# Optimization experiments

Hardware: AMD Instinct MI355X
Metric: run time of the kernel (lower is better)

## Reference

```python
import jax, jax.numpy as jnp
import numpy as np

B, S, H = 1, 2048, 4096
NH, NKV, HD = 32, 8, 128
GROUP = NH // NKV  # 4
SCALE = 0.08838834764831845  # 1/sqrt(head_dim)
ROPE_BASE = 10000.0


def setup_inputs() -> dict:
    key = jax.random.key(0)
    k1, k2, k3 = jax.random.split(key, 3)
    hidden_states = jax.random.normal(k1, (B, S, H), jnp.float32)
    # c_attn: [H + 2*NKV*HD, H] = [6144, 4096]; c_proj: [H, H]
    w_attn = jax.random.normal(k2, (H + 2 * NKV * HD, H), jnp.float32) * 0.02
    w_proj = jax.random.normal(k3, (H, H), jnp.float32) * (0.02 / np.sqrt(2 * 32))
    # standard rotate-half RoPE tables, shape [S, HD]
    inv_freq = 1.0 / (ROPE_BASE ** (jnp.arange(0, HD, 2, dtype=jnp.float32) / HD))
    freqs = jnp.outer(jnp.arange(S, dtype=jnp.float32), inv_freq)
    emb = jnp.concatenate([freqs, freqs], axis=-1)
    return {
        "hidden_states": hidden_states,
        "w_attn": w_attn,
        "w_proj": w_proj,
        "rope_cos": jnp.cos(emb),
        "rope_sin": jnp.sin(emb),
    }


def _apply_rope(x, cos, sin):
    # x: [B, heads, S, HD]; cos/sin: [S, HD] broadcast over batch/heads
    x1, x2 = jnp.split(x, 2, axis=-1)
    rot = jnp.concatenate([-x2, x1], axis=-1)
    return x * cos + rot * sin


def reference(hidden_states, w_attn, w_proj, rope_cos, rope_sin):
    b, s, _ = hidden_states.shape
    # fused QKV projection (no bias)
    qkv = hidden_states @ w_attn.T  # [B, S, H + 2*NKV*HD]
    qkv = qkv.reshape(b, s, NKV, (GROUP + 2) * HD)
    q = qkv[..., : GROUP * HD].reshape(b, s, NH, HD)
    k = qkv[..., GROUP * HD : (GROUP + 1) * HD]  # [B, S, NKV, HD]
    v = qkv[..., (GROUP + 1) * HD :]
    q = q.transpose(0, 2, 1, 3)  # [B, NH, S, HD]
    k = k.transpose(0, 2, 1, 3)  # [B, NKV, S, HD]
    v = v.transpose(0, 2, 1, 3)
    q = _apply_rope(q, rope_cos, rope_sin)
    k = _apply_rope(k, rope_cos, rope_sin)
    # GQA: group query heads per kv head instead of repeating K/V
    qg = q.reshape(b, NKV, GROUP, s, HD)
    scores = jnp.einsum("bkgqd,bksd->bkgqs", qg, k) * SCALE
    causal = jnp.tril(jnp.ones((s, s), dtype=bool))
    scores = jnp.where(causal, scores, jnp.finfo(scores.dtype).min)
    probs = jax.nn.softmax(scores, axis=-1)
    out = jnp.einsum("bkgqs,bksd->bkgqd", probs, v)
    out = out.reshape(b, NH, s, HD).transpose(0, 2, 1, 3).reshape(b, s, NH * HD)
    return out @ w_proj.T
```

## Files before the change

kernel.cpp:

```cpp
#include <hip/hip_runtime.h>
#include <cstdint>
#include <cstddef>

typedef __attribute__((ext_vector_type(4))) float f32x4;
typedef __attribute__((ext_vector_type(8))) short bf16x8;

#define S_LEN 2048
#define HDIM 4096
#define QKVD 6144
#define NHEAD 32
#define NKVH 8
#define HD 128
#define ATT_SCALE 0.08838834764831845f

__device__ __forceinline__ short f2bf(float f) {
  unsigned int u = __float_as_uint(f);
  u += 0x7FFFu + ((u >> 16) & 1u);
  return (short)(u >> 16);
}

__device__ __forceinline__ void gl_lds16(const short* g, short* l) {
  __builtin_amdgcn_global_load_lds((const __attribute__((address_space(1))) void*)g,
                                   (__attribute__((address_space(3))) void*)l,
                                   16, 0, 0);
}

template<int N> __device__ __forceinline__ void vmw() {
  if constexpr (N == 0) asm volatile("s_waitcnt vmcnt(0)" ::: "memory");
  else if constexpr (N == 1) asm volatile("s_waitcnt vmcnt(1)" ::: "memory");
  else if constexpr (N == 2) asm volatile("s_waitcnt vmcnt(2)" ::: "memory");
  else if constexpr (N == 3) asm volatile("s_waitcnt vmcnt(3)" ::: "memory");
  else if constexpr (N == 4) asm volatile("s_waitcnt vmcnt(4)" ::: "memory");
}

__global__ void cvt_kernel(const float* __restrict__ in, short* __restrict__ out, int n) {
  int i = (blockIdx.x * blockDim.x + threadIdx.x) * 4;
  if (i >= n) return;
  const float4 v = *reinterpret_cast<const float4*>(in + i);
  short4 o;
  o.x = f2bf(v.x); o.y = f2bf(v.y); o.z = f2bf(v.z); o.w = f2bf(v.w);
  *reinterpret_cast<short4*>(out + i) = o;
}

#define PHASEX(MH, NH, VM, STAGE) { \
    bf16x8 af[2][2], bfr[NQ][2]; \
    { const short* bA = lA + buf * ATILE; const short* bB = lB + buf * BTILE; \
      _Pragma("unroll") for (int m = 0; m < 2; ++m) { \
        int row = wm * 64 + (MH) * 32 + m * 16 + l15; \
        _Pragma("unroll") for (int kk = 0; kk < 2; ++kk) { \
          int slot = ((kk << 2) + l4) ^ (row & 7); \
          af[m][kk] = *reinterpret_cast<const bf16x8*>(bA + row * 64 + slot * 8); } } \
      _Pragma("unroll") for (int n = 0; n < NQ; ++n) { \
        int row = wn * (BN >> 2) + n * 32 + (NH) * 16 + l15; \
        _Pragma("unroll") for (int kk = 0; kk < 2; ++kk) { \
          int slot = ((kk << 2) + l4) ^ (row & 7); \
          bfr[n][kk] = *reinterpret_cast<const bf16x8*>(bB + row * 64 + slot * 8); } } } \
    STAGE; \
    vmw<(VM)>(); \
    __builtin_amdgcn_s_barrier(); \
    __builtin_amdgcn_sched_barrier(0); \
    __builtin_amdgcn_s_setprio(1); \
    _Pragma("unroll") for (int m = 0; m < 2; ++m) \
      _Pragma("unroll") for (int n = 0; n < NQ; ++n) \
        _Pragma("unroll") for (int kk = 0; kk < 2; ++kk) \
          acc[(MH) * 2 + m][(NH) * NQ + n] = __builtin_amdgcn_mfma_f32_16x16x32_bf16( \
              af[m][kk], bfr[n][kk], acc[(MH) * 2 + m][(NH) * NQ + n], 0, 0, 0); \
    __builtin_amdgcn_s_setprio(0); }

template<int BN>
__global__ __launch_bounds__(512, 2) void gemm8p(const short* __restrict__ A,
                                                 const short* __restrict__ B,
                                                 float* __restrict__ C,
                                                 int M, int N, int K) {
  extern __shared__ short sm[];
  constexpr int NQ = BN / 128;
  constexpr int ATILE = 128 * 64;
  constexpr int BTILE = BN * 64;
  const int tid = threadIdx.x;
  const int wv = tid >> 6, lane = tid & 63;
  const int wm = wv >> 2, wn = wv & 3;
  const int l15 = lane & 15, l4 = lane >> 4;
  const int nbn = N / BN;
  const int nwg = gridDim.x;
  const int bid = blockIdx.x;
  const int sbid = (bid & 7) * (nwg >> 3) + (bid >> 3);
  const int tm = (sbid / nbn) * 128, tn = (sbid % nbn) * BN;
  short* lA = sm;
  short* lB = sm + 2 * ATILE;
  (void)M;

  f32x4 acc[4][2 * NQ] = {};

  auto stageA = [&](int k0, int bufi, int sel) {
    short* dst = lA + bufi * ATILE;
    int rowIdx = tid >> 3;
    int row = (rowIdx >> 5) * 64 + sel * 32 + (rowIdx & 31);
    int slot = tid & 7;
    gl_lds16(A + (size_t)(tm + row) * K + k0 + ((slot ^ (row & 7)) << 3),
             dst + row * 64 + slot * 8);
  };
  auto stageB = [&](int k0, int bufi, int par) {
    short* dst = lB + bufi * BTILE;
#pragma unroll
    for (int j = 0; j < NQ; ++j) {
      int rowIdx = (tid >> 3) + j * 64;
      int row = (rowIdx >> 4) * 32 + par * 16 + (rowIdx & 15);
      int slot = tid & 7;
      gl_lds16(B + (size_t)(tn + row) * K + k0 + ((slot ^ (row & 7)) << 3),
               dst + row * 64 + slot * 8);
    }
  };

  stageA(0, 0, 0);
  stageB(0, 0, 0);
  stageB(0, 0, 1);
  stageA(0, 0, 1);
  vmw<NQ + 1>();
  __builtin_amdgcn_s_barrier();
  __builtin_amdgcn_sched_barrier(0);

  const int KT = K >> 6;
  for (int t = 0; t < KT - 1; ++t) {
    const int buf = t & 1, nbuf = buf ^ 1, nk0 = (t + 1) << 6;
    PHASEX(0, 0, 2,      stageA(nk0, nbuf, 0))
    PHASEX(0, 1, NQ + 1, stageB(nk0, nbuf, 0))
    PHASEX(1, 0, 99,     stageB(nk0, nbuf, 1))
    PHASEX(1, 1, NQ + 1, stageA(nk0, nbuf, 1))
  }
  {
    const int buf = (KT - 1) & 1;
    PHASEX(0, 0, 1,  (void)0)
    PHASEX(0, 1, 0,  (void)0)
    PHASEX(1, 0, 99, (void)0)
    PHASEX(1, 1, 99, (void)0)
  }
#pragma unroll
  for (int mg = 0; mg < 4; ++mg)
#pragma unroll
    for (int NH = 0; NH < 2; ++NH)
#pragma unroll
      for (int n = 0; n < NQ; ++n)
#pragma unroll
        for (int r = 0; r < 4; ++r) {
          int row = tm + wm * 64 + mg * 16 + l4 * 4 + r;
          int col = tn + wn * (BN >> 2) + n * 32 + NH * 16 + l15;
          C[(size_t)row * N + col] = acc[mg][NH * NQ + n][r];
        }
}

__global__ void rope2_kernel(const float* __restrict__ qkv,
                             const float* __restrict__ cb,
                             const float* __restrict__ sb,
                             short* __restrict__ Q,
                             short* __restrict__ Kx) {
  int tid = blockIdx.x * blockDim.x + threadIdx.x;
  int dh = tid & 63;
  int t2 = tid >> 6;
  int part = t2 % 5;
  int t3 = t2 / 5;
  int g = t3 & 7;
  int s = t3 >> 3;
  const float* base = qkv + (size_t)s * QKVD + g * 768 + part * 128;
  float v1 = base[dh], v2 = base[dh + 64];
  float c = cb[s * HD + dh], sn = sb[s * HD + dh];
  float o1 = v1 * c - v2 * sn;
  float o2 = v2 * c + v1 * sn;
  short* dst = (part < 4) ? (Q + ((size_t)(g * 4 + part) * S_LEN + s) * HD)
                          : (Kx + ((size_t)g * S_LEN + s) * HD);
  dst[dh] = f2bf(o1);
  dst[dh + 64] = f2bf(o2);
}

__global__ __launch_bounds__(256) void vtrans2_kernel(const float* __restrict__ qkv,
                                                      short* __restrict__ Vt) {
  __shared__ short tile[64][72];
  const int kvh = blockIdx.z;
  const int s0 = blockIdx.x * 64, d0 = blockIdx.y * 64;
  const int t = threadIdx.x;
#pragma unroll
  for (int i = 0; i < 4; ++i) {
    int c = t + i * 256;
    int sl = c >> 4, dl = (c & 15) * 4;
    const float4 v = *reinterpret_cast<const float4*>(
        qkv + (size_t)(s0 + sl) * QKVD + kvh * 768 + 640 + d0 + dl);
    tile[sl][dl] = f2bf(v.x); tile[sl][dl + 1] = f2bf(v.y);
    tile[sl][dl + 2] = f2bf(v.z); tile[sl][dl + 3] = f2bf(v.w);
  }
  __syncthreads();
  short* Vtb = Vt + (size_t)kvh * HD * S_LEN;
#pragma unroll
  for (int i = 0; i < 2; ++i) {
    int dl = i * 32 + (t >> 3), sl = (t & 7) * 8;
    bf16x8 o;
#pragma unroll
    for (int j = 0; j < 8; ++j) o[j] = tile[sl + j][dl];
    *reinterpret_cast<bf16x8*>(Vtb + (size_t)(d0 + dl) * S_LEN + s0 + sl) = o;
  }
}

__global__ __launch_bounds__(256, 2) void attn_kernel(const short* __restrict__ Q,
                                                      const short* __restrict__ Kx,
                                                      const short* __restrict__ Vt,
                                                      short* __restrict__ AO) {
  __shared__ short lK[2 * 64 * 128];
  __shared__ unsigned int lPu[4 * 2 * 512];
  const int tt = threadIdx.x;
  const int w = tt >> 6, lane = tt & 63;
  const int l15 = lane & 15, l4 = lane >> 4;
  const int kvh = blockIdx.x;
  const int y = blockIdx.y;
  const int qt = (y < 32) ? (2 * y) : (127 - 2 * y);
  const int h = kvh * 4 + w;

  bf16x8 qf[2][4];
#pragma unroll
  for (int qa = 0; qa < 2; ++qa) {
    const short* qrow = Q + ((size_t)h * S_LEN + qt * 32 + qa * 16 + l15) * HD + l4 * 8;
#pragma unroll
    for (int fd = 0; fd < 4; ++fd)
      qf[qa][fd] = *reinterpret_cast<const bf16x8*>(qrow + fd * 32);
  }

  f32x4 o[2][8] = {};
  float m_run[2] = {-1e30f, -1e30f};
  float lsum[2] = {0.f, 0.f};

  const short* Kb = Kx + (size_t)kvh * S_LEN * HD;
  const short* Vb = Vt + (size_t)kvh * HD * S_LEN;
  const int nkt = (qt >> 1) + 1;

#pragma unroll
  for (int i = 0; i < 4; ++i) {
    int c = tt + i * 256, row = c >> 4, jj = (c & 15) ^ (row & 7);
    gl_lds16(Kb + (size_t)row * HD + jj * 8, lK + c * 8);
  }
  __syncthreads();

  int cur = 0;
  for (int kt = 0; kt < nkt; ++kt) {
    const int c0 = kt * 64;
    if (kt + 1 < nkt) {
      const short* Kg = Kb + (size_t)(c0 + 64) * HD;
      short* dst = lK + (cur ^ 1) * (64 * 128);
#pragma unroll
      for (int i = 0; i < 4; ++i) {
        int c = tt + i * 256, row = c >> 4, jj = (c & 15) ^ (row & 7);
        gl_lds16(Kg + (size_t)row * HD + jj * 8, dst + c * 8);
      }
    }
    const short* src = lK + cur * (64 * 128);
    f32x4 sf[2][4] = {};
    __builtin_amdgcn_s_setprio(1);
#pragma unroll
    for (int n = 0; n < 4; ++n) {
      bf16x8 kf[4];
#pragma unroll
      for (int fd = 0; fd < 4; ++fd) {
        int row = n * 16 + l15, jp = (l4 + fd * 4) ^ (l15 & 7);
        kf[fd] = *reinterpret_cast<const bf16x8*>(src + row * 128 + jp * 8);
      }
#pragma unroll
      for (int fd = 0; fd < 4; ++fd) {
        sf[0][n] = __builtin_amdgcn_mfma_f32_16x16x32_bf16(kf[fd], qf[0][fd], sf[0][n], 0, 0, 0);
        sf[1][n] = __builtin_amdgcn_mfma_f32_16x16x32_bf16(kf[fd], qf[1][fd], sf[1][n], 0, 0, 0);
      }
    }
    __builtin_amdgcn_s_setprio(0);
    bf16x8 vreg[8][2];
#pragma unroll
    for (int fd = 0; fd < 8; ++fd) {
      const short* vrow = Vb + (size_t)(fd * 16 + l15) * S_LEN + c0 + l4 * 8;
      vreg[fd][0] = *reinterpret_cast<const bf16x8*>(vrow);
      vreg[fd][1] = *reinterpret_cast<const bf16x8*>(vrow + 32);
    }
    const bool lastt = (kt == nkt - 1);
#pragma unroll
    for (int qa = 0; qa < 2; ++qa) {
      const int qrow_g = qt * 32 + qa * 16 + l15;
#pragma unroll
      for (int n = 0; n < 4; ++n)
#pragma unroll
        for (int r = 0; r < 4; ++r) {
          float v = sf[qa][n][r] * ATT_SCALE;
          if (lastt && (c0 + n * 16 + l4 * 4 + r) > qrow_g) v = -1e30f;
          sf[qa][n][r] = v;
        }
      float mx = sf[qa][0][0];
#pragma unroll
      for (int n = 0; n < 4; ++n)
#pragma unroll
        for (int r = 0; r < 4; ++r) mx = fmaxf(mx, sf[qa][n][r]);
      mx = fmaxf(mx, __shfl_xor(mx, 16, 64));
      mx = fmaxf(mx, __shfl_xor(mx, 32, 64));
      float mnew = fmaxf(m_run[qa], mx);
      float alpha = __expf(m_run[qa] - mnew);
      m_run[qa] = mnew;
      float ps = 0.f;
#pragma unroll
      for (int n = 0; n < 4; ++n)
#pragma unroll
        for (int r = 0; r < 4; ++r) {
          float e = __expf(sf[qa][n][r] - mnew);
          sf[qa][n][r] = e;
          ps += e;
        }
      lsum[qa] = lsum[qa] * alpha + ps;
#pragma unroll
      for (int n = 0; n < 4; ++n)
#pragma unroll
        for (int rp = 0; rp < 2; ++rp) {
          unsigned int pkv =
              ((unsigned int)(unsigned short)f2bf(sf[qa][n][rp * 2 + 1]) << 16) |
              (unsigned short)f2bf(sf[qa][n][rp * 2]);
          int kv5 = ((n & 1) << 4) + l4 * 4 + rp * 2;
          lPu[w * 1024 + qa * 512 + ((n >> 1) << 8) +
              (l15 + ((kv5 >> 3) << 4)) * 4 + ((kv5 & 7) >> 1)] = pkv;
        }
      float aO[4];
#pragma unroll
      for (int r = 0; r < 4; ++r) aO[r] = __shfl(alpha, l4 * 4 + r, 64);
#pragma unroll
      for (int fd = 0; fd < 8; ++fd) {
        o[qa][fd][0] *= aO[0]; o[qa][fd][1] *= aO[1];
        o[qa][fd][2] *= aO[2]; o[qa][fd][3] *= aO[3];
      }
    }
    asm volatile("s_waitcnt lgkmcnt(0)" ::: "memory");
    bf16x8 pf[2][2];
#pragma unroll
    for (int qa = 0; qa < 2; ++qa)
#pragma unroll
      for (int p = 0; p < 2; ++p)
        pf[qa][p] = *reinterpret_cast<const bf16x8*>(
            (const short*)lPu + (w * 1024 + qa * 512 + p * 256 + lane * 4) * 2);
    __builtin_amdgcn_s_setprio(1);
#pragma unroll
    for (int fd = 0; fd < 8; ++fd) {
      o[0][fd] = __builtin_amdgcn_mfma_f32_16x16x32_bf16(pf[0][0], vreg[fd][0], o[0][fd], 0, 0, 0);
      o[0][fd] = __builtin_amdgcn_mfma_f32_16x16x32_bf16(pf[0][1], vreg[fd][1], o[0][fd], 0, 0, 0);
      o[1][fd] = __builtin_amdgcn_mfma_f32_16x16x32_bf16(pf[1][0], vreg[fd][0], o[1][fd], 0, 0, 0);
      o[1][fd] = __builtin_amdgcn_mfma_f32_16x16x32_bf16(pf[1][1], vreg[fd][1], o[1][fd], 0, 0, 0);
    }
    __builtin_amdgcn_s_setprio(0);
    __syncthreads();
    cur ^= 1;
  }
#pragma unroll
  for (int qa = 0; qa < 2; ++qa) {
    float s = lsum[qa];
    s += __shfl_xor(s, 16, 64);
    s += __shfl_xor(s, 32, 64);
    float inv = 1.f / s;
    float iO[4];
#pragma unroll
    for (int r = 0; r < 4; ++r) iO[r] = __shfl(inv, l4 * 4 + r, 64);
#pragma unroll
    for (int fd = 0; fd < 8; ++fd)
#pragma unroll
      for (int r = 0; r < 4; ++r)
        AO[(size_t)(qt * 32 + qa * 16 + l4 * 4 + r) * HDIM + h * HD + fd * 16 + l15] =
            f2bf(o[qa][fd][r] * iO[r]);
  }
}

extern "C" void kernel_launch(void* const* d_in, const int* in_sizes, int n_in,
                              void* d_out, int out_size, void* d_ws, size_t ws_size,
                              hipStream_t stream) {
  const float* hidden = (const float*)d_in[0];
  const float* w_attn = (const float*)d_in[1];
  const float* w_proj = (const float*)d_in[2];
  const float* rcos = (const float*)d_in[3];
  const float* rsin = (const float*)d_in[4];
  float* out = (float*)d_out;
  char* ws = (char*)d_ws;

  short* Xb  = (short*)(ws);
  short* Wab = (short*)(ws + (16u << 20));
  short* Qb  = (short*)(ws + (16u << 20));
  short* Kb  = (short*)(ws + (32u << 20));
  short* Vtb = (short*)(ws + (40u << 20));
  float* QKVf = (float*)(ws + (64u << 20));
  short* Wpb = (short*)(ws + (64u << 20));
  short* AO  = Xb;

  const int nX = S_LEN * HDIM;
  const int nWa = QKVD * HDIM;
  const int nWp = HDIM * HDIM;

  hipFuncSetAttribute(reinterpret_cast<const void*>(gemm8p<384>),
                      hipFuncAttributeMaxDynamicSharedMemorySize, 131072);
  hipFuncSetAttribute(reinterpret_cast<const void*>(gemm8p<256>),
                      hipFuncAttributeMaxDynamicSharedMemorySize, 98304);

  cvt_kernel<<<nX / 1024, 256, 0, stream>>>(hidden, Xb, nX);
  cvt_kernel<<<nWa / 1024, 256, 0, stream>>>(w_attn, Wab, nWa);
  gemm8p<384><<<256, 512, 131072, stream>>>(Xb, Wab, QKVf, S_LEN, QKVD, HDIM);
  rope2_kernel<<<(S_LEN * NKVH * 5 * 64) / 256, 256, 0, stream>>>(QKVf, rcos, rsin, Qb, Kb);
  vtrans2_kernel<<<dim3(S_LEN / 64, HD / 64, NKVH), 256, 0, stream>>>(QKVf, Vtb);
  cvt_kernel<<<nWp / 1024, 256, 0, stream>>>(w_proj, Wpb, nWp);
  attn_kernel<<<dim3(NKVH, 64), 256, 0, stream>>>(Qb, Kb, Vtb, AO);
  gemm8p<256><<<256, 512, 98304, stream>>>(AO, Wpb, out, S_LEN, HDIM, HDIM);
}
```

Before: 353.0 us.

## Split attention KV range across two blocks and merge with combine kernel

Splits each query tile's causal KV loop into two halves processed by separate blocks (grid z=2). Each block writes unnormalised partial outputs plus (max, sum) stats, and a new combine kernel merges them into AO. This doubles parallelism and evens out load across the causal triangle. It also folds the softmax scale and log2(e) into Q in the rope kernel so the softmax can use exp2f without a per-score multiply. The cost is extra bf16 partial-output traffic, an extra kernel launch, and a second bf16 rounding of the partials.

Result: no change. 346.5 us (-1.8%).

```diff
diff --git a/kernel.cpp b/kernel.cpp
--- a/kernel.cpp
+++ b/kernel.cpp
@@ -11,12 +11,15 @@
 #define NHEAD 32
 #define NKVH 8
 #define HD 128
-#define ATT_SCALE 0.08838834764831845f
+#define QPRE 0.12751744631123533f
 
 __device__ __forceinline__ short f2bf(float f) {
   unsigned int u = __float_as_uint(f);
   u += 0x7FFFu + ((u >> 16) & 1u);
   return (short)(u >> 16);
+}
+__device__ __forceinline__ float bf2f(short s) {
+  return __uint_as_float((unsigned int)(unsigned short)s << 16);
 }
 
 __device__ __forceinline__ void gl_lds16(const short* g, short* l) {
@@ -165,10 +168,16 @@
   float c = cb[s * HD + dh], sn = sb[s * HD + dh];
   float o1 = v1 * c - v2 * sn;
   float o2 = v2 * c + v1 * sn;
-  short* dst = (part < 4) ? (Q + ((size_t)(g * 4 + part) * S_LEN + s) * HD)
-                          : (Kx + ((size_t)g * S_LEN + s) * HD);
-  dst[dh] = f2bf(o1);
-  dst[dh + 64] = f2bf(o2);
+  if (part < 4) {
+    o1 *= QPRE; o2 *= QPRE;
+    short* dst = Q + ((size_t)(g * 4 + part) * S_LEN + s) * HD;
+    dst[dh] = f2bf(o1);
+    dst[dh + 64] = f2bf(o2);
+  } else {
+    short* dst = Kx + ((size_t)g * S_LEN + s) * HD;
+    dst[dh] = f2bf(o1);
+    dst[dh + 64] = f2bf(o2);
+  }
 }
 
 __global__ __launch_bounds__(256) void vtrans2_kernel(const float* __restrict__ qkv,
@@ -201,166 +210,200 @@
 __global__ __launch_bounds__(256, 2) void attn_kernel(const short* __restrict__ Q,
                                                       const short* __restrict__ Kx,
                                                       const short* __restrict__ Vt,
-                                                      short* __restrict__ AO) {
+                                                      short* __restrict__ part0,
+                                                      short* __restrict__ part1,
+                                                      float2* __restrict__ stat0,
+                                                      float2* __restrict__ stat1) {
   __shared__ short lK[2 * 64 * 128];
   __shared__ unsigned int lPu[4 * 2 * 512];
   const int tt = threadIdx.x;
   const int w = tt >> 6, lane = tt & 63;
   const int l15 = lane & 15, l4 = lane >> 4;
   const int kvh = blockIdx.x;
-  const int y = blockIdx.y;
-  const int qt = (y < 32) ? (2 * y) : (127 - 2 * y);
+  const int qt = 63 - blockIdx.y;
+  const int z = blockIdx.z;
   const int h = kvh * 4 + w;
-
-  bf16x8 qf[2][4];
-#pragma unroll
-  for (int qa = 0; qa < 2; ++qa) {
-    const short* qrow = Q + ((size_t)h * S_LEN + qt * 32 + qa * 16 + l15) * HD + l4 * 8;
-#pragma unroll
-    for (int fd = 0; fd < 4; ++fd)
-      qf[qa][fd] = *reinterpret_cast<const bf16x8*>(qrow + fd * 32);
-  }
+  short* pout = z ? part1 : part0;
+  float2* sout = z ? stat1 : stat0;
+
+  const int nkt = (qt >> 1) + 1;
+  const int ts = (nkt + 1) >> 1;
+  const int t0 = z ? ts : 0;
+  const int t1 = z ? nkt : ts;
 
   f32x4 o[2][8] = {};
   float m_run[2] = {-1e30f, -1e30f};
   float lsum[2] = {0.f, 0.f};
 
-  const short* Kb = Kx + (size_t)kvh * S_LEN * HD;
-  const short* Vb = Vt + (size_t)kvh * HD * S_LEN;
-  const int nkt = (qt >> 1) + 1;
-
-#pragma unroll
-  for (int i = 0; i < 4; ++i) {
-    int c = tt + i * 256, row = c >> 4, jj = (c & 15) ^ (row & 7);
-    gl_lds16(Kb + (size_t)row * HD + jj * 8, lK + c * 8);
-  }
-  __syncthreads();
-
-  int cur = 0;
-  for (int kt = 0; kt < nkt; ++kt) {
-    const int c0 = kt * 64;
-    if (kt + 1 < nkt) {
-      const short* Kg = Kb + (size_t)(c0 + 64) * HD;
-      short* dst = lK + (cur ^ 1) * (64 * 128);
+  if (t0 < t1) {
+    bf16x8 qf[2][4];
+#pragma unroll
+    for (int qa = 0; qa < 2; ++qa) {
+      const short* qrow = Q + ((size_t)h * S_LEN + qt * 32 + qa * 16 + l15) * HD + l4 * 8;
+#pragma unroll
+      for (int fd = 0; fd < 4; ++fd)
+        qf[qa][fd] = *reinterpret_cast<const bf16x8*>(qrow + fd * 32);
+    }
+    const short* Kb = Kx + (size_t)kvh * S_LEN * HD;
+    const short* Vb = Vt + (size_t)kvh * HD * S_LEN;
+
+    {
+      const short* Kg = Kb + (size_t)(t0 * 64) * HD;
 #pragma unroll
       for (int i = 0; i < 4; ++i) {
         int c = tt + i * 256, row = c >> 4, jj = (c & 15) ^ (row & 7);
-        gl_lds16(Kg + (size_t)row * HD + jj * 8, dst + c * 8);
+        gl_lds16(Kg + (size_t)row * HD + jj * 8, lK + c * 8);
       }
     }
-    const short* src = lK + cur * (64 * 128);
-    f32x4 sf[2][4] = {};
-    __builtin_amdgcn_s_setprio(1);
-#pragma unroll
-    for (int n = 0; n < 4; ++n) {
-      bf16x8 kf[4];
-#pragma unroll
-      for (int fd = 0; fd < 4; ++fd) {
-        int row = n * 16 + l15, jp = (l4 + fd * 4) ^ (l15 & 7);
-        kf[fd] = *reinterpret_cast<const bf16x8*>(src + row * 128 + jp * 8);
-      }
-#pragma unroll
-      for (int fd = 0; fd < 4; ++fd) {
-        sf[0][n] = __builtin_amdgcn_mfma_f32_16x16x32_bf16(kf[fd], qf[0][fd], sf[0][n], 0, 0, 0);
-        sf[1][n] = __builtin_amdgcn_mfma_f32_16x16x32_bf16(kf[fd], qf[1][fd], sf[1][n], 0, 0, 0);
-      }
+    __syncthreads();
+
+    int cur = 0;
+    for (int kt = t0; kt < t1; ++kt) {
+      const int c0 = kt * 64;
+      if (kt + 1 < t1) {
+        const short* Kg = Kb + (size_t)(c0 + 64) * HD;
+        short* dst = lK + (cur ^ 1) * (64 * 128);
+#pragma unroll
+        for (int i = 0; i < 4; ++i) {
+          int c = tt + i * 256, row = c >> 4, jj = (c & 15) ^ (row & 7);
+          gl_lds16(Kg + (size_t)row * HD + jj * 8, dst + c * 8);
+        }
+      }
+      const short* src = lK + cur * (64 * 128);
+      f32x4 sf[2][4] = {};
+      __builtin_amdgcn_s_setprio(1);
+#pragma unroll
+      for (int n = 0; n < 4; ++n) {
+        bf16x8 kf[4];
+#pragma unroll
+        for (int fd = 0; fd < 4; ++fd) {
+          int row = n * 16 + l15, jp = (l4 + fd * 4) ^ (l15 & 7);
+          kf[fd] = *reinterpret_cast<const bf16x8*>(src + row * 128 + jp * 8);
+        }
+#pragma unroll
+        for (int fd = 0; fd < 4; ++fd) {
+          sf[0][n] = __builtin_amdgcn_mfma_f32_16x16x32_bf16(kf[fd], qf[0][fd], sf[0][n], 0, 0, 0);
+          sf[1][n] = __builtin_amdgcn_mfma_f32_16x16x32_bf16(kf[fd], qf[1][fd], sf[1][n], 0, 0, 0);
+        }
+      }
+      __builtin_amdgcn_s_setprio(0);
+      bf16x8 vreg[8][2];
+#pragma unroll
+      for (int fd = 0; fd < 8; ++fd) {
+        const short* vrow = Vb + (size_t)(fd * 16 + l15) * S_LEN + c0 + l4 * 8;
+        vreg[fd][0] = *reinterpret_cast<const bf16x8*>(vrow);
+        vreg[fd][1] = *reinterpret_cast<const bf16x8*>(vrow + 32);
+      }
+      const bool lastt = (kt == nkt - 1);
+#pragma unroll
+      for (int qa = 0; qa < 2; ++qa) {
+        if (lastt) {
+          const int qrow_g = qt * 32 + qa * 16 + l15;
+#pragma unroll
+          for (int n = 0; n < 4; ++n)
+#pragma unroll
+            for (int r = 0; r < 4; ++r)
+              if ((c0 + n * 16 + l4 * 4 + r) > qrow_g) sf[qa][n][r] = -1e30f;
+        }
+        float mx = sf[qa][0][0];
+#pragma unroll
+        for (int n = 0; n < 4; ++n)
+#pragma unroll
+          for (int r = 0; r < 4; ++r) mx = fmaxf(mx, sf[qa][n][r]);
+        mx = fmaxf(mx, __shfl_xor(mx, 16, 64));
+        mx = fmaxf(mx, __shfl_xor(mx, 32, 64));
+        float mnew = fmaxf(m_run[qa], mx);
+        float alpha = exp2f(m_run[qa] - mnew);
+        m_run[qa] = mnew;
+        float ps = 0.f;
+#pragma unroll
+        for (int n = 0; n < 4; ++n)
+#pragma unroll
+          for (int r = 0; r < 4; ++r) {
+            float e = exp2f(sf[qa][n][r] - mnew);
+            sf[qa][n][r] = e;
+            ps += e;
+          }
+        lsum[qa] = lsum[qa] * alpha + ps;
+#pragma unroll
+        for (int n = 0; n < 4; ++n)
+#pragma unroll
+          for (int rp = 0; rp < 2; ++rp) {
+            unsigned int pkv =
+                ((unsigned int)(unsigned short)f2bf(sf[qa][n][rp * 2 + 1]) << 16) |
+                (unsigned short)f2bf(sf[qa][n][rp * 2]);
+            int kv5 = ((n & 1) << 4) + l4 * 4 + rp * 2;
+            lPu[w * 1024 + qa * 512 + ((n >> 1) << 8) +
+                (l15 + ((kv5 >> 3) << 4)) * 4 + ((kv5 & 7) >> 1)] = pkv;
+          }
+        float aO[4];
+#pragma unroll
+        for (int r = 0; r < 4; ++r) aO[r] = __shfl(alpha, l4 * 4 + r, 64);
+#pragma unroll
+        for (int fd = 0; fd < 8; ++fd) {
+          o[qa][fd][0] *= aO[0]; o[qa][fd][1] *= aO[1];
+          o[qa][fd][2] *= aO[2]; o[qa][fd][3] *= aO[3];
+        }
+      }
+      asm volatile("s_waitcnt lgkmcnt(0)" ::: "memory");
+      bf16x8 pf[2][2];
+#pragma unroll
+      for (int qa = 0; qa < 2; ++qa)
+#pragma unroll
+        for (int p = 0; p < 2; ++p)
+          pf[qa][p] = *reinterpret_cast<const bf16x8*>(
+              (const short*)lPu + (w * 1024 + qa * 512 + p * 256 + lane * 4) * 2);
+      __builtin_amdgcn_s_setprio(1);
+#pragma unroll
+      for (int fd = 0; fd < 8; ++fd) {
+        o[0][fd] = __builtin_amdgcn_mfma_f32_16x16x32_bf16(pf[0][0], vreg[fd][0], o[0][fd], 0, 0, 0);
+        o[0][fd] = __builtin_amdgcn_mfma_f32_16x16x32_bf16(pf[0][1], vreg[fd][1], o[0][fd], 0, 0, 0);
+        o[1][fd] = __builtin_amdgcn_mfma_f32_16x16x32_bf16(pf[1][0], vreg[fd][0], o[1][fd], 0, 0, 0);
+        o[1][fd] = __builtin_amdgcn_mfma_f32_16x16x32_bf16(pf[1][1], vreg[fd][1], o[1][fd], 0, 0, 0);
+      }
+      __builtin_amdgcn_s_setprio(0);
+      __syncthreads();
+      cur ^= 1;
     }
-    __builtin_amdgcn_s_setprio(0);
-    bf16x8 vreg[8][2];
-#pragma unroll
-    for (int fd = 0; fd < 8; ++fd) {
-      const short* vrow = Vb + (size_t)(fd * 16 + l15) * S_LEN + c0 + l4 * 8;
-      vreg[fd][0] = *reinterpret_cast<const bf16x8*>(vrow);
-      vreg[fd][1] = *reinterpret_cast<const bf16x8*>(vrow + 32);
-    }
-    const bool lastt = (kt == nkt - 1);
-#pragma unroll
-    for (int qa = 0; qa < 2; ++qa) {
-      const int qrow_g = qt * 32 + qa * 16 + l15;
-#pragma unroll
-      for (int n = 0; n < 4; ++n)
-#pragma unroll
-        for (int r = 0; r < 4; ++r) {
-          float v = sf[qa][n][r] * ATT_SCALE;
-          if (lastt && (c0 + n * 16 + l4 * 4 + r) > qrow_g) v = -1e30f;
-          sf[qa][n][r] = v;
-        }
-      float mx = sf[qa][0][0];
-#pragma unroll
-      for (int n = 0; n < 4; ++n)
-#pragma unroll
-        for (int r = 0; r < 4; ++r) mx = fmaxf(mx, sf[qa][n][r]);
-      mx = fmaxf(mx, __shfl_xor(mx, 16, 64));
-      mx = fmaxf(mx, __shfl_xor(mx, 32, 64));
-      float mnew = fmaxf(m_run[qa], mx);
-      float alpha = __expf(m_run[qa] - mnew);
-      m_run[qa] = mnew;
-      float ps = 0.f;
-#pragma unroll
-      for (int n = 0; n < 4; ++n)
-#pragma unroll
-        for (int r = 0; r < 4; ++r) {
-          float e = __expf(sf[qa][n][r] - mnew);
-          sf[qa][n][r] = e;
-          ps += e;
-        }
-      lsum[qa] = lsum[qa] * alpha + ps;
-#pragma unroll
-      for (int n = 0; n < 4; ++n)
-#pragma unroll
-        for (int rp = 0; rp < 2; ++rp) {
-          unsigned int pkv =
-              ((unsigned int)(unsigned short)f2bf(sf[qa][n][rp * 2 + 1]) << 16) |
-              (unsigned short)f2bf(sf[qa][n][rp * 2]);
-          int kv5 = ((n & 1) << 4) + l4 * 4 + rp * 2;
-          lPu[w * 1024 + qa * 512 + ((n >> 1) << 8) +
-              (l15 + ((kv5 >> 3) << 4)) * 4 + ((kv5 & 7) >> 1)] = pkv;
-        }
-      float aO[4];
-#pragma unroll
-      for (int r = 0; r < 4; ++r) aO[r] = __shfl(alpha, l4 * 4 + r, 64);
-#pragma unroll
-      for (int fd = 0; fd < 8; ++fd) {
-        o[qa][fd][0] *= aO[0]; o[qa][fd][1] *= aO[1];
-        o[qa][fd][2] *= aO[2]; o[qa][fd][3] *= aO[3];
-      }
-    }
-    asm volatile("s_waitcnt lgkmcnt(0)" ::: "memory");
-    bf16x8 pf[2][2];
-#pragma unroll
-    for (int qa = 0; qa < 2; ++qa)
-#pragma unroll
-      for (int p = 0; p < 2; ++p)
-        pf[qa][p] = *reinterpret_cast<const bf16x8*>(
-            (const short*)lPu + (w * 1024 + qa * 512 + p * 256 + lane * 4) * 2);
-    __builtin_amdgcn_s_setprio(1);
-#pragma unroll
-    for (int fd = 0; fd < 8; ++fd) {
-      o[0][fd] = __builtin_amdgcn_mfma_f32_16x16x32_bf16(pf[0][0], vreg[fd][0], o[0][fd], 0, 0, 0);
-      o[0][fd] = __builtin_amdgcn_mfma_f32_16x16x32_bf16(pf[0][1], vreg[fd][1], o[0][fd], 0, 0, 0);
-      o[1][fd] = __builtin_amdgcn_mfma_f32_16x16x32_bf16(pf[1][0], vreg[fd][0], o[1][fd], 0, 0, 0);
-      o[1][fd] = __builtin_amdgcn_mfma_f32_16x16x32_bf16(pf[1][1], vreg[fd][1], o[1][fd], 0, 0, 0);
-    }
-    __builtin_amdgcn_s_setprio(0);
-    __syncthreads();
-    cur ^= 1;
   }
 #pragma unroll
   for (int qa = 0; qa < 2; ++qa) {
     float s = lsum[qa];
     s += __shfl_xor(s, 16, 64);
     s += __shfl_xor(s, 32, 64);
-    float inv = 1.f / s;
-    float iO[4];
-#pragma unroll
-    for (int r = 0; r < 4; ++r) iO[r] = __shfl(inv, l4 * 4 + r, 64);
+    if (l4 == 0)
+      sout[(size_t)h * S_LEN + qt * 32 + qa * 16 + l15] = make_float2(m_run[qa], s);
 #pragma unroll
     for (int fd = 0; fd < 8; ++fd)
 #pragma unroll
       for (int r = 0; r < 4; ++r)
-        AO[(size_t)(qt * 32 + qa * 16 + l4 * 4 + r) * HDIM + h * HD + fd * 16 + l15] =
-            f2bf(o[qa][fd][r] * iO[r]);
-  }
+        pout[((size_t)h * S_LEN + qt * 32 + qa * 16 + l4 * 4 + r) * HD + fd * 16 + l15] =
+            f2bf(o[qa][fd][r]);
+  }
+}
+
+__global__ __launch_bounds__(256) void combine_kernel(const short* __restrict__ p0,
+                                                      const short* __restrict__ p1,
+                                                      const float2* __restrict__ st0,
+                                                      const float2* __restrict__ st1,
+                                                      short* __restrict__ AO) {
+  int idx = (blockIdx.x * 256 + threadIdx.x) * 8;
+  int h = idx >> 18;
+  int rem = idx & ((1 << 18) - 1);
+  int s = rem >> 7, d = rem & 127;
+  float2 a = st0[(size_t)h * S_LEN + s];
+  float2 b = st1[(size_t)h * S_LEN + s];
+  float M = fmaxf(a.x, b.x);
+  float w0 = exp2f(a.x - M), w1 = exp2f(b.x - M);
+  float inv = 1.f / (a.y * w0 + b.y * w1);
+  w0 *= inv; w1 *= inv;
+  bf16x8 v0 = *reinterpret_cast<const bf16x8*>(p0 + idx);
+  bf16x8 v1 = *reinterpret_cast<const bf16x8*>(p1 + idx);
+  bf16x8 ov;
+#pragma unroll
+  for (int j = 0; j < 8; ++j)
+    ov[j] = f2bf(bf2f(v0[j]) * w0 + bf2f(v1[j]) * w1);
+  *reinterpret_cast<bf16x8*>(AO + (size_t)s * HDIM + h * HD + d) = ov;
 }
 
 extern "C" void kernel_launch(void* const* d_in, const int* in_sizes, int n_in,
@@ -379,8 +422,12 @@
   short* Qb  = (short*)(ws + (16u << 20));
   short* Kb  = (short*)(ws + (32u << 20));
   short* Vtb = (short*)(ws + (40u << 20));
+  short* Pt0 = (short*)(ws + (44u << 20));
+  float2* St0 = (float2*)(ws + (60u << 20));
+  float2* St1 = (float2*)(ws + (61u << 20));
   float* QKVf = (float*)(ws + (64u << 20));
   short* Wpb = (short*)(ws + (64u << 20));
+  short* Pt1 = (short*)(ws + (96u << 20));
   short* AO  = Xb;
 
   const int nX = S_LEN * HDIM;
@@ -398,6 +445,7 @@
   rope2_kernel<<<(S_LEN * NKVH * 5 * 64) / 256, 256, 0, stream>>>(QKVf, rcos, rsin, Qb, Kb);
   vtrans2_kernel<<<dim3(S_LEN / 64, HD / 64, NKVH), 256, 0, stream>>>(QKVf, Vtb);
   cvt_kernel<<<nWp / 1024, 256, 0, stream>>>(w_proj, Wpb, nWp);
-  attn_kernel<<<dim3(NKVH, 64), 256, 0, stream>>>(Qb, Kb, Vtb, AO);
+  attn_kernel<<<dim3(NKVH, 64, 2), 256, 0, stream>>>(Qb, Kb, Vtb, Pt0, Pt1, St0, St1);
+  combine_kernel<<<(NHEAD * S_LEN * HD / 8) / 256, 256, 0, stream>>>(Pt0, Pt1, St0, St1, AO);
   gemm8p<256><<<256, 512, 98304, stream>>>(AO, Wpb, out, S_LEN, HDIM, HDIM);
 }
```
